# Performance work log

Measured on AMD Instinct MI355X. Metric: run time of the kernel, lower is better.

The kernel has to match this reference:

```python
import jax, jax.numpy as jnp
import numpy as np

J, XD, HD, YD, P, N = 64, 512, 1024, 16, 8, 1024


def setup_inputs() -> dict:
    key = jax.random.key(0)
    ks = jax.random.split(key, 14)
    b1 = 2.0 / np.sqrt(XD)
    b2 = 2.0 / np.sqrt(HD)
    rng = np.random.RandomState(0)
    # stack of P permutation matrices [P, YD, YD]
    permu = jnp.asarray(np.stack([np.eye(YD, dtype=np.float32)[rng.permutation(YD)] for _ in range(P)]))
    return {
        "x": jax.random.normal(ks[0], (N, XD), jnp.float32),
        "mu_W1": b1 * (jax.random.uniform(ks[1], (XD, HD)) - 0.5),
        "mu_b1": b1 * (jax.random.uniform(ks[2], (1, HD)) - 0.5),
        "mu_W2": b2 * (jax.random.uniform(ks[3], (HD, YD)) - 0.5),
        "mu_b2": b2 * (jax.random.uniform(ks[4], (1, YD)) - 0.5),
        "sig_W1": b1 * jax.random.uniform(ks[5], (XD, HD)),
        "sig_b1": b1 * jax.random.uniform(ks[6], (1, HD)),
        "sig_W2": b2 * jax.random.uniform(ks[7], (HD, YD)),
        "sig_b2": b2 * jax.random.uniform(ks[8], (1, YD)),
        "e_W1": jax.random.normal(ks[9], (J, XD, HD), jnp.float32),
        "e_b1": jax.random.normal(ks[10], (J, 1, HD), jnp.float32),
        "e_W2": jax.random.normal(ks[11], (J, HD, YD), jnp.float32),
        "e_b2": jax.random.normal(ks[12], (J, 1, YD), jnp.float32),
        "permu": permu,
    }


def reference(x, mu_W1, mu_b1, mu_W2, mu_b2, sig_W1, sig_b1, sig_W2, sig_b2,
              e_W1, e_b1, e_W2, e_b2, permu):
    # reparameterized weight samples: [J, ...]
    W1 = mu_W1 + e_W1 * sig_W1          # [J, XD, HD]
    b1 = mu_b1 + e_b1 * sig_b1          # [J, 1, HD]
    W2 = mu_W2 + e_W2 * sig_W2          # [J, HD, YD]
    b2 = mu_b2 + e_b2 * sig_b2          # [J, 1, YD]
    xf = x.reshape(-1, XD)
    # Hardtanh(-1, 1) == clip
    h = jnp.clip(jnp.einsum('nx,jxh->jnh', xf, W1) + b1, -1.0, 1.0)  # [J, N, HD]
    out = jnp.einsum('jnh,jhy->jny', h, W2) + b2                      # [J, N, YD]
    all_out = jnp.einsum('jnc,pcy->jpny', out, permu)                 # [J, P, N, YD]
    return all_out.reshape(J * P, xf.shape[0], YD)
```

## Files before the change

kernel.cpp:

```cpp
#include <hip/hip_runtime.h>
#include <cstdint>
#include <cstddef>

#define J 64
#define XD 512
#define HD 1024
#define YD 16
#define PP 8
#define NN 1024

typedef __bf16 bf16;
typedef __attribute__((ext_vector_type(8))) __bf16 bf16x8;
typedef __attribute__((ext_vector_type(4))) __bf16 bf16x4;
typedef __attribute__((ext_vector_type(4))) float f32x4;

__device__ __forceinline__ void gload16(const void* g, void* l) {
  __builtin_amdgcn_global_load_lds((__attribute__((address_space(1))) void*)(g),
                                   (__attribute__((address_space(3))) void*)(l),
                                   16, 0, 0);
}

__global__ __launch_bounds__(256) void build_all(
    const float* __restrict__ muW1, const float* __restrict__ sigW1,
    const float* __restrict__ eW1, bf16* __restrict__ W1T,
    const float* __restrict__ x,
    const float* __restrict__ muW2, const float* __restrict__ sigW2,
    const float* __restrict__ eW2,
    const float* __restrict__ mub1, const float* __restrict__ sigb1,
    const float* __restrict__ eb1,
    const float* __restrict__ mub2, const float* __restrict__ sigb2,
    const float* __restrict__ eb2,
    bf16* __restrict__ XBF, bf16* __restrict__ W2T,
    float* __restrict__ B1W, float* __restrict__ B2W) {
  __shared__ bf16 sT[64][66];
  int b = blockIdx.x;
  int tid = threadIdx.x;
  if (b < 8192) {
    int j = b >> 7;
    int xt = (b >> 4) & 7;
    int ht = b & 15;
    int x0 = xt << 6, h0 = ht << 6;
    int rp = tid >> 4;
    int cp = (tid & 15) << 2;
    const float* eB = eW1 + (size_t)j * (XD * HD);
#pragma unroll
    for (int p = 0; p < 4; ++p) {
      int xx = rp + (p << 4);
      size_t gi = (size_t)(x0 + xx) * HD + (h0 + cp);
      f32x4 e = *(const f32x4*)(eB + gi);
      f32x4 m = *(const f32x4*)(muW1 + gi);
      f32x4 s = *(const f32x4*)(sigW1 + gi);
#pragma unroll
      for (int i = 0; i < 4; ++i) sT[cp + i][xx] = (bf16)(m[i] + e[i] * s[i]);
    }
    __syncthreads();
#pragma unroll
    for (int p = 0; p < 4; ++p) {
      int h = rp + (p << 4);
      bf16x4 v;
#pragma unroll
      for (int i = 0; i < 4; ++i) v[i] = sT[h][cp + i];
      *(bf16x4*)(W1T + (size_t)(j * HD + h0 + h) * XD + (x0 + cp)) = v;
    }
    return;
  }
  int i = (b - 8192) * 256 + tid;
  const int c0 = NN * XD;
  const int c1 = J * YD * HD;
  const int c2 = J * HD;
  const int c3 = J * YD;
  if (i < c0) { XBF[i] = (bf16)x[i]; return; }
  i -= c0;
  if (i < c1) {
    int h = i & (HD - 1);
    int jy = i >> 10;
    int y = jy & 15;
    int j = jy >> 4;
    float mu = muW2[h * YD + y], sg = sigW2[h * YD + y];
    float e = eW2[((size_t)j * HD + h) * YD + y];
    W2T[i] = (bf16)(mu + e * sg);
    return;
  }
  i -= c1;
  if (i < c2) {
    int h = i & (HD - 1);
    B1W[i] = mub1[h] + eb1[i] * sigb1[h];
    return;
  }
  i -= c2;
  if (i < c3) {
    int y = i & 15;
    B2W[i] = mub2[y] + eb2[i] * sigb2[y];
  }
}

__global__ __launch_bounds__(512)
__attribute__((amdgpu_waves_per_eu(2, 2)))
void fused_mlp(
    const bf16* __restrict__ XBF, const bf16* __restrict__ W1T,
    const bf16* __restrict__ W2T, const float* __restrict__ B1W,
    const float* __restrict__ B2W, const float* __restrict__ permu,
    float* __restrict__ out) {
  extern __shared__ char smem[];

  int bid = blockIdx.x;
  int L = ((bid & 7) << 5) | (bid >> 3);
  int j = L >> 2;
  int n0 = (L & 3) << 8;

  int tid = threadIdx.x;
  int wid = tid >> 6;
  int lane = tid & 63;
  int l15 = lane & 15;
  int lg = lane >> 4;
  int wn = (wid >> 1) << 6;
  int wh = (wid & 1) << 6;
  int srow = tid >> 3;
  int slot = tid & 7;

  const bf16* w1base = W1T + (size_t)j * (HD * XD);
  const bf16* w2g = W2T + (size_t)((j << 4) + l15) * HD;
  bf16* sH = (bf16*)(smem + 98304);

  f32x4 acc2[2];
#pragma unroll
  for (int f = 0; f < 2; ++f)
#pragma unroll
    for (int r = 0; r < 4; ++r) acc2[f][r] = 0.0f;

  auto stage = [&](int d, int k0, int hb_) {
    char* aD = smem + d * 32768 + (tid << 4);
    char* bD = smem + 65536 + d * 16384 + (tid << 4);
#pragma unroll
    for (int q = 0; q < 4; ++q) {
      int r = (q << 6) + srow;
      int sc = slot ^ (r & 7);
      gload16(XBF + (size_t)(n0 + r) * XD + k0 + (sc << 3), aD + (q << 13));
      if (q < 2)
        gload16(w1base + (size_t)((hb_ << 7) + r) * XD + k0 + (sc << 3), bD + (q << 13));
    }
  };

  stage(0, 0, 0);
  asm volatile("s_waitcnt vmcnt(0)" ::: "memory");
  __builtin_amdgcn_s_barrier();

#pragma unroll 1
  for (int hb = 0; hb < 8; ++hb) {
    f32x4 acc1[4][4];
#pragma unroll
    for (int fb = 0; fb < 4; ++fb)
#pragma unroll
      for (int fa = 0; fa < 4; ++fa)
#pragma unroll
        for (int r = 0; r < 4; ++r) acc1[fb][fa][r] = 0.0f;

    int cur = 0;
#pragma unroll 1
    for (int t = 0; t < 8; ++t) {
      const char* a_d = smem + cur * 32768;
      const char* b_d = smem + 65536 + cur * 16384;
#pragma unroll
      for (int kk = 0; kk < 2; ++kk) {
        bf16x8 af[4], bg[4];
#pragma unroll
        for (int fa = 0; fa < 4; ++fa) {
          int ra = wn + (fa << 4) + l15;
          int ca = ((kk << 6) + (lg << 4)) ^ ((ra & 7) << 4);
          af[fa] = *(const bf16x8*)(a_d + (ra << 7) + ca);
        }
#pragma unroll
        for (int fb = 0; fb < 4; ++fb) {
          int rb = wh + (fb << 4) + l15;
          int cb = ((kk << 6) + (lg << 4)) ^ ((rb & 7) << 4);
          bg[fb] = *(const bf16x8*)(b_d + (rb << 7) + cb);
        }
        if (kk == 0) {
          if (t < 7)            stage(cur ^ 1, (t + 1) << 6, hb);
          else if (hb < 7)      stage(cur ^ 1, 0, hb + 1);
        }
        __builtin_amdgcn_s_setprio(1);
#pragma unroll
        for (int fb = 0; fb < 4; ++fb)
#pragma unroll
          for (int fa = 0; fa < 4; ++fa)
            acc1[fb][fa] = __builtin_amdgcn_mfma_f32_16x16x32_bf16(
                bg[fb], af[fa], acc1[fb][fa], 0, 0, 0);
        __builtin_amdgcn_s_setprio(0);
      }
      asm volatile("s_waitcnt vmcnt(0)" ::: "memory");
      __builtin_amdgcn_s_barrier();
      cur ^= 1;
    }

    bf16x8 wg[4];
#pragma unroll
    for (int kk2 = 0; kk2 < 4; ++kk2)
      wg[kk2] = *(const bf16x8*)(w2g + (hb << 7) + (kk2 << 5) + (lg << 3));

    f32x4 b1v[4];
#pragma unroll
    for (int fb = 0; fb < 4; ++fb)
      b1v[fb] = *(const f32x4*)&B1W[(j << 10) + (hb << 7) + wh + (fb << 4) + (lg << 2)];
#pragma unroll
    for (int fa = 0; fa < 4; ++fa) {
#pragma unroll
      for (int fb = 0; fb < 4; ++fb) {
        bf16x4 pk;
#pragma unroll
        for (int r = 0; r < 4; ++r) {
          float v = acc1[fb][fa][r] + b1v[fb][r];
          v = fminf(1.0f, fmaxf(-1.0f, v));
          pk[r] = (bf16)v;
        }
        int n = wn + (fa << 4) + l15;
        int colb = (wh + (fb << 4) + (lg << 2)) << 1;
        int byte = (n << 8) + (colb ^ ((n & 7) << 4));
        *(bf16x4*)((char*)sH + byte) = pk;
      }
    }
    asm volatile("s_waitcnt lgkmcnt(0)" ::: "memory");
    __builtin_amdgcn_s_barrier();
#pragma unroll
    for (int kk2 = 0; kk2 < 4; ++kk2) {
#pragma unroll
      for (int f = 0; f < 2; ++f) {
        int row = (wid << 5) + (f << 4) + l15;
        int cb = ((kk2 << 6) + (lg << 4)) ^ ((row & 7) << 4);
        bf16x8 hf = *(const bf16x8*)((char*)sH + (row << 8) + cb);
        acc2[f] = __builtin_amdgcn_mfma_f32_16x16x32_bf16(hf, wg[kk2], acc2[f], 0, 0, 0);
      }
    }
  }

  float b2v = B2W[(j << 4) + l15];
  float* sOut = (float*)smem;
  int* sIdx = (int*)(smem + 20480);
#pragma unroll
  for (int f = 0; f < 2; ++f)
#pragma unroll
    for (int r = 0; r < 4; ++r) {
      int row = (wid << 5) + (f << 4) + (lg << 2) + r;
      sOut[row * 17 + l15] = acc2[f][r] + b2v;
    }
  if (tid < 128) {
    int p = tid >> 4, y = tid & 15;
    int c = 0;
#pragma unroll
    for (int cc = 0; cc < 16; ++cc)
      if (permu[((p << 4) + cc) * 16 + y] > 0.5f) c = cc;
    sIdx[tid] = c;
  }
  __syncthreads();
#pragma unroll 1
  for (int it = 0; it < 16; ++it) {
    int flat = (it << 11) + (tid << 2);
    int p = flat >> 12;
    int n = (flat >> 4) & 255;
    int y0 = flat & 15;
    f32x4 v;
#pragma unroll
    for (int q = 0; q < 4; ++q) v[q] = sOut[n * 17 + sIdx[(p << 4) + y0 + q]];
    *(f32x4*)(out + ((size_t)((j << 3) + p) * NN + n0 + n) * YD + y0) = v;
  }
}

extern "C" void kernel_launch(void* const* d_in, const int* in_sizes, int n_in,
                              void* d_out, int out_size, void* d_ws, size_t ws_size,
                              hipStream_t stream) {
  (void)in_sizes; (void)n_in; (void)out_size; (void)ws_size;
  const float* x      = (const float*)d_in[0];
  const float* mu_W1  = (const float*)d_in[1];
  const float* mu_b1  = (const float*)d_in[2];
  const float* mu_W2  = (const float*)d_in[3];
  const float* mu_b2  = (const float*)d_in[4];
  const float* sig_W1 = (const float*)d_in[5];
  const float* sig_b1 = (const float*)d_in[6];
  const float* sig_W2 = (const float*)d_in[7];
  const float* sig_b2 = (const float*)d_in[8];
  const float* e_W1   = (const float*)d_in[9];
  const float* e_b1   = (const float*)d_in[10];
  const float* e_W2   = (const float*)d_in[11];
  const float* e_b2   = (const float*)d_in[12];
  const float* permu  = (const float*)d_in[13];
  float* out = (float*)d_out;

  char* ws = (char*)d_ws;
  bf16* W1T = (bf16*)(ws);
  bf16* W2T = (bf16*)(ws + 67108864);
  bf16* XBF = (bf16*)(ws + 69206016);
  float* B1W = (float*)(ws + 70254592);
  float* B2W = (float*)(ws + 70516736);

  static int lds_set = 0;
  if (!lds_set) {
    hipFuncSetAttribute((const void*)fused_mlp,
                        hipFuncAttributeMaxDynamicSharedMemorySize, 163840);
    lds_set = 1;
  }

  build_all<<<dim3(14596), dim3(256), 0, stream>>>(
      mu_W1, sig_W1, e_W1, W1T,
      x, mu_W2, sig_W2, e_W2, mu_b1, sig_b1, e_b1, mu_b2, sig_b2, e_b2,
      XBF, W2T, B1W, B2W);
  fused_mlp<<<dim3(256), dim3(512), 163840, stream>>>(
      XBF, W1T, W2T, B1W, B2W, permu, out);
}
```

Baseline: 119.3 us.

## Halve fused MLP tile to 128 rows with 256-thread blocks and smaller LDS

Switches the fused MLP kernel from 256 blocks of 512 threads (256 rows × 128 hidden per tile, 160KB LDS) to 512 blocks of 256 threads (128 rows per tile, 64KB LDS). The H staging buffer now aliases the A/B double buffers, so the prefetch of the next hidden block moves after the second GEMM, with extra barriers. The aim is more blocks per CU and better occupancy across the 256 CUs. The cost is less reuse of W1 per block, twice the W1 traffic, and a serialized load at each hidden-block boundary.

```diff
diff --git a/kernel.cpp b/kernel.cpp
--- a/kernel.cpp
+++ b/kernel.cpp
@@ -94,8 +94,7 @@
   }
 }
 
-__global__ __launch_bounds__(512)
-__attribute__((amdgpu_waves_per_eu(2, 2)))
+__global__ __launch_bounds__(256)
 void fused_mlp(
     const bf16* __restrict__ XBF, const bf16* __restrict__ W1T,
     const bf16* __restrict__ W2T, const float* __restrict__ B1W,
@@ -104,9 +103,9 @@
   extern __shared__ char smem[];
 
   int bid = blockIdx.x;
-  int L = ((bid & 7) << 5) | (bid >> 3);
-  int j = L >> 2;
-  int n0 = (L & 3) << 8;
+  int L = ((bid & 7) << 6) | (bid >> 3);
+  int j = L >> 3;
+  int n0 = (L & 7) << 7;
 
   int tid = threadIdx.x;
   int wid = tid >> 6;
@@ -115,12 +114,10 @@
   int lg = lane >> 4;
   int wn = (wid >> 1) << 6;
   int wh = (wid & 1) << 6;
-  int srow = tid >> 3;
-  int slot = tid & 7;
 
   const bf16* w1base = W1T + (size_t)j * (HD * XD);
   const bf16* w2g = W2T + (size_t)((j << 4) + l15) * HD;
-  bf16* sH = (bf16*)(smem + 98304);
+  bf16* sH = (bf16*)smem;
 
   f32x4 acc2[2];
 #pragma unroll
@@ -129,15 +126,15 @@
     for (int r = 0; r < 4; ++r) acc2[f][r] = 0.0f;
 
   auto stage = [&](int d, int k0, int hb_) {
-    char* aD = smem + d * 32768 + (tid << 4);
-    char* bD = smem + 65536 + d * 16384 + (tid << 4);
 #pragma unroll
     for (int q = 0; q < 4; ++q) {
-      int r = (q << 6) + srow;
-      int sc = slot ^ (r & 7);
-      gload16(XBF + (size_t)(n0 + r) * XD + k0 + (sc << 3), aD + (q << 13));
-      if (q < 2)
-        gload16(w1base + (size_t)((hb_ << 7) + r) * XD + k0 + (sc << 3), bD + (q << 13));
+      int r = (q << 5) + (tid >> 3);
+      int sc = (tid & 7) ^ (r & 7);
+      int doff = (q << 12) + (tid << 4);
+      gload16(XBF + (size_t)(n0 + r) * XD + k0 + (sc << 3),
+              smem + d * 16384 + doff);
+      gload16(w1base + (size_t)((hb_ << 7) + r) * XD + k0 + (sc << 3),
+              smem + 32768 + d * 16384 + doff);
     }
   };
 
@@ -155,11 +152,11 @@
 #pragma unroll
         for (int r = 0; r < 4; ++r) acc1[fb][fa][r] = 0.0f;
 
-    int cur = 0;
 #pragma unroll 1
     for (int t = 0; t < 8; ++t) {
-      const char* a_d = smem + cur * 32768;
-      const char* b_d = smem + 65536 + cur * 16384;
+      int cur = t & 1;
+      const char* a_d = smem + cur * 16384;
+      const char* b_d = smem + 32768 + cur * 16384;
 #pragma unroll
       for (int kk = 0; kk < 2; ++kk) {
         bf16x8 af[4], bg[4];
@@ -175,10 +172,7 @@
           int cb = ((kk << 6) + (lg << 4)) ^ ((rb & 7) << 4);
           bg[fb] = *(const bf16x8*)(b_d + (rb << 7) + cb);
         }
-        if (kk == 0) {
-          if (t < 7)            stage(cur ^ 1, (t + 1) << 6, hb);
-          else if (hb < 7)      stage(cur ^ 1, 0, hb + 1);
-        }
+        if (kk == 0 && t < 7) stage(cur ^ 1, (t + 1) << 6, hb);
         __builtin_amdgcn_s_setprio(1);
 #pragma unroll
         for (int fb = 0; fb < 4; ++fb)
@@ -190,7 +184,6 @@
       }
       asm volatile("s_waitcnt vmcnt(0)" ::: "memory");
       __builtin_amdgcn_s_barrier();
-      cur ^= 1;
     }
 
     bf16x8 wg[4];
@@ -231,11 +224,18 @@
         acc2[f] = __builtin_amdgcn_mfma_f32_16x16x32_bf16(hf, wg[kk2], acc2[f], 0, 0, 0);
       }
     }
-  }
-
+    if (hb < 7) {
+      __builtin_amdgcn_s_barrier();
+      stage(0, 0, hb + 1);
+      asm volatile("s_waitcnt vmcnt(0)" ::: "memory");
+      __builtin_amdgcn_s_barrier();
+    }
+  }
+
+  __syncthreads();
   float b2v = B2W[(j << 4) + l15];
   float* sOut = (float*)smem;
-  int* sIdx = (int*)(smem + 20480);
+  int* sIdx = (int*)(smem + 12288);
 #pragma unroll
   for (int f = 0; f < 2; ++f)
 #pragma unroll
@@ -254,9 +254,9 @@
   __syncthreads();
 #pragma unroll 1
   for (int it = 0; it < 16; ++it) {
-    int flat = (it << 11) + (tid << 2);
-    int p = flat >> 12;
-    int n = (flat >> 4) & 255;
+    int flat = (it << 10) + (tid << 2);
+    int p = flat >> 11;
+    int n = (flat >> 4) & 127;
     int y0 = flat & 15;
     f32x4 v;
 #pragma unroll
@@ -292,17 +292,10 @@
   float* B1W = (float*)(ws + 70254592);
   float* B2W = (float*)(ws + 70516736);
 
-  static int lds_set = 0;
-  if (!lds_set) {
-    hipFuncSetAttribute((const void*)fused_mlp,
-                        hipFuncAttributeMaxDynamicSharedMemorySize, 163840);
-    lds_set = 1;
-  }
-
   build_all<<<dim3(14596), dim3(256), 0, stream>>>(
       mu_W1, sig_W1, e_W1, W1T,
       x, mu_W2, sig_W2, e_W2, mu_b1, sig_b1, e_b1, mu_b2, sig_b2, e_b2,
       XBF, W2T, B1W, B2W);
-  fused_mlp<<<dim3(256), dim3(512), 163840, stream>>>(
+  fused_mlp<<<dim3(512), dim3(256), 65536, stream>>>(
       XBF, W1T, W2T, B1W, B2W, permu, out);
 }
```

Result: slower. 161.5 us (+35.4%).
